# Performance work log

Measured on AMD Instinct MI355X. Metric: run time of the kernel, lower is better.

Reference implementation:

```python
import jax, jax.numpy as jnp
import numpy as np


def setup_inputs() -> dict:
    key = jax.random.key(0)
    k1, k2, k3, k4 = jax.random.split(key, 4)
    B, N, M, D = 4, 4096, 4096, 64
    x = jax.random.normal(k1, (B, N, D), dtype=jnp.float32)
    y = jax.random.normal(k2, (B, M, D), dtype=jnp.float32)
    mu = jax.random.normal(k3, (D, 1), dtype=jnp.float32)
    logs2diag = jax.random.normal(k4, (D,), dtype=jnp.float32) * 0.1
    return {"x": x, "y": y, "mu": mu, "logs2diag": logs2diag}


def reference(x, y, mu, logs2diag):
    # Diagonal scaling: x_ = x @ diag(exp(logs2diag)**0.5) == x * s_sqrt (broadcast)
    s_sqrt = jnp.exp(0.5 * logs2diag)  # [D]
    x_ = x * s_sqrt  # [B,N,D]
    y_ = y * s_sqrt  # [B,M,D]
    # cos term: M = x@mu - (y@mu)^T  -> [B,N,M]
    m_x = jnp.einsum('bnd,dk->bnk', x, mu)  # [B,N,1]
    m_y = jnp.einsum('bmd,dk->bmk', y, mu)  # [B,M,1]
    Mdiff = m_x - jnp.swapaxes(m_y, 1, 2)   # [B,N,M]
    # squared euclidean distance without sqrt (exp(-0.5*cdist^2))
    x2 = jnp.sum(x_ * x_, axis=-1, keepdims=True)      # [B,N,1]
    y2 = jnp.sum(y_ * y_, axis=-1, keepdims=True)      # [B,M,1]
    xy = jnp.einsum('bnd,bmd->bnm', x_, y_)            # [B,N,M]
    sqd = jnp.maximum(x2 + jnp.swapaxes(y2, 1, 2) - 2.0 * xy, 0.0)
    return jnp.cos(Mdiff) * jnp.exp(-0.5 * sqd)
```

## Files before the change

kernel.cpp:

```cpp
#include <hip/hip_runtime.h>
#include <math.h>

typedef __attribute__((ext_vector_type(8))) short short8;
typedef __attribute__((ext_vector_type(4))) float f32x4;

constexpr int D    = 64;
constexpr int BT_N = 64;
constexpr int BT_M = 512;
constexpr int NSUB = 8;

__device__ inline float fastcos_rev(float r) {
#if __has_builtin(__builtin_amdgcn_cosf)
    return __builtin_amdgcn_cosf(r);
#else
    return __cosf(r * 6.283185307179586f);
#endif
}
__device__ inline float fastsin_rev(float r) {
#if __has_builtin(__builtin_amdgcn_sinf)
    return __builtin_amdgcn_sinf(r);
#else
    return __sinf(r * 6.283185307179586f);
#endif
}

__device__ inline void split8(const float* v, short8& hi, short8& lo) {
    #pragma unroll
    for (int j = 0; j < 8; ++j) {
        unsigned u = __builtin_bit_cast(unsigned, v[j]);
        hi[j] = (short)(u >> 16);
        float hf = __builtin_bit_cast(float, u & 0xffff0000u);
        float r  = v[j] - hf;
        lo[j] = (short)(__builtin_bit_cast(unsigned, r) >> 16);
    }
}

__device__ inline void split1(float f, short& hi, short& lo) {
    unsigned u = __builtin_bit_cast(unsigned, f);
    hi = (short)(u >> 16);
    float hf = __builtin_bit_cast(float, u & 0xffff0000u);
    lo = (short)(__builtin_bit_cast(unsigned, f - hf) >> 16);
}

__global__ __launch_bounds__(256) void prep_kernel(
    const float* __restrict__ x, const float* __restrict__ y,
    const float* __restrict__ mu, const float* __restrict__ ls2,
    unsigned short* __restrict__ xh, unsigned short* __restrict__ xl,
    unsigned short* __restrict__ yh, unsigned short* __restrict__ yl,
    float4* __restrict__ xst, float4* __restrict__ yst,
    int BN, int BM)
{
    __shared__ float ss[D], sm[D];
    const int t = threadIdx.x;
    if (t < D) { ss[t] = __expf(0.5f * ls2[t]); sm[t] = mu[t]; }
    __syncthreads();

    const int gid = blockIdx.x * 256 + t;
    const int row = gid >> 3;
    const int sub = gid & 7;
    if (row >= BN + BM) return;

    const float* src;
    unsigned short *ph, *pl;
    float4* pst;
    int r;
    if (row < BN) { r = row;      src = x + (size_t)r * D; ph = xh; pl = xl; pst = xst; }
    else          { r = row - BN; src = y + (size_t)r * D; ph = yh; pl = yl; pst = yst; }

    const int k0 = sub * 8;
    float4 u0 = *(const float4*)(src + k0);
    float4 u1 = *(const float4*)(src + k0 + 4);
    const float4 m0 = *(const float4*)&sm[k0];
    const float4 m1 = *(const float4*)&sm[k0 + 4];
    const float4 s0 = *(const float4*)&ss[k0];
    const float4 s1 = *(const float4*)&ss[k0 + 4];

    float m = u0.x*m0.x + u0.y*m0.y + u0.z*m0.z + u0.w*m0.w
            + u1.x*m1.x + u1.y*m1.y + u1.z*m1.z + u1.w*m1.w;
    u0.x *= s0.x; u0.y *= s0.y; u0.z *= s0.z; u0.w *= s0.w;
    u1.x *= s1.x; u1.y *= s1.y; u1.z *= s1.z; u1.w *= s1.w;
    float h = u0.x*u0.x + u0.y*u0.y + u0.z*u0.z + u0.w*u0.w
            + u1.x*u1.x + u1.y*u1.y + u1.z*u1.z + u1.w*u1.w;

    m += __shfl_xor(m, 1); m += __shfl_xor(m, 2); m += __shfl_xor(m, 4);
    h += __shfl_xor(h, 1); h += __shfl_xor(h, 2); h += __shfl_xor(h, 4);

    if (sub == 0) {
        constexpr float INV2PI = 0.15915494309189535f;
        float rr = m * INV2PI;
        rr -= floorf(rr);
        pst[r] = (float4){0.5f * h, fastcos_rev(rr), fastsin_rev(rr), 0.f};
    }

    float v[8] = {u0.x, u0.y, u0.z, u0.w, u1.x, u1.y, u1.z, u1.w};
    short8 hi, lo;
    split8(v, hi, lo);
    const size_t o = (size_t)(r >> 4) * 1024 + (size_t)(sub * 16 + (r & 15)) * 8;
    *(short8*)(ph + o) = hi;
    *(short8*)(pl + o) = lo;
}

__device__ __forceinline__ void load_b(
    short8 (&bh)[2][2], short8 (&bl)[2][2],
    const unsigned short* __restrict__ ybh, const unsigned short* __restrict__ ybl,
    int st)
{
    #pragma unroll
    for (int kc = 0; kc < 2; ++kc)
        #pragma unroll
        for (int j = 0; j < 2; ++j) {
            const size_t o = (size_t)st * 4096 + j * 1024 + kc * 512;
            bh[kc][j] = *(const short8*)(ybh + o);
            bl[kc][j] = *(const short8*)(ybl + o);
        }
}

__device__ __forceinline__ void compute_store(
    const short8 (&ah)[2][2], const short8 (&al)[2][2],
    const short8 (&exA)[2],
    const short8 (&bh)[2][2], const short8 (&bl)[2][2],
    const float4* __restrict__ stB,
    const float (&say)[2][4], const float (&saz)[2][4],
    float* __restrict__ outb, int M, int st, int wc, int l15, int lg)
{
    short8 exB[2];
    #pragma unroll
    for (int j = 0; j < 2; ++j) {
        const float hy = -stB[st * 64 + wc * 32 + j * 16 + l15].x;
        short hh, hl;
        split1(hy, hh, hl);
        short8 v = (short8){0,0,0,0,0,0,0,0};
        if (lg == 0) { v[0] = (short)0x3f80; v[1] = (short)0x3f80; v[2] = hh; v[3] = hl; }
        exB[j] = v;
    }

    f32x4 acc[2][2];
    #pragma unroll
    for (int i = 0; i < 2; ++i)
        #pragma unroll
        for (int j = 0; j < 2; ++j)
            acc[i][j] = (f32x4){0.f, 0.f, 0.f, 0.f};

    #pragma unroll
    for (int kc = 0; kc < 2; ++kc)
        #pragma unroll
        for (int i = 0; i < 2; ++i)
            #pragma unroll
            for (int j = 0; j < 2; ++j) {
                acc[i][j] = __builtin_amdgcn_mfma_f32_16x16x32_bf16(ah[kc][i], bh[kc][j], acc[i][j], 0, 0, 0);
                acc[i][j] = __builtin_amdgcn_mfma_f32_16x16x32_bf16(ah[kc][i], bl[kc][j], acc[i][j], 0, 0, 0);
                acc[i][j] = __builtin_amdgcn_mfma_f32_16x16x32_bf16(al[kc][i], bh[kc][j], acc[i][j], 0, 0, 0);
            }
    #pragma unroll
    for (int i = 0; i < 2; ++i)
        #pragma unroll
        for (int j = 0; j < 2; ++j)
            acc[i][j] = __builtin_amdgcn_mfma_f32_16x16x32_bf16(exA[i], exB[j], acc[i][j], 0, 0, 0);

    const float4 sb0 = stB[st * 64 + wc * 32 + l15];
    const float4 sb1 = stB[st * 64 + wc * 32 + 16 + l15];
    #pragma unroll
    for (int i = 0; i < 2; ++i)
        #pragma unroll
        for (int q = 0; q < 4; ++q) {
            {
                const float cv = say[i][q] * sb0.y + saz[i][q] * sb0.z;
                outb[(size_t)(i * 16 + q) * M + st * 64] = cv * __expf(acc[i][0][q]);
            }
            {
                const float cv = say[i][q] * sb1.y + saz[i][q] * sb1.z;
                outb[(size_t)(i * 16 + q) * M + st * 64 + 16] = cv * __expf(acc[i][1][q]);
            }
        }
}

__global__ __launch_bounds__(256) void main_kernel(
    const unsigned short* __restrict__ xh, const unsigned short* __restrict__ xl,
    const unsigned short* __restrict__ yh, const unsigned short* __restrict__ yl,
    const float4* __restrict__ xst, const float4* __restrict__ yst,
    float* __restrict__ out, int N, int M)
{
    __shared__ float4 stA[BT_N], stB[BT_M];

    const int b  = blockIdx.z;
    const int n0 = blockIdx.y * BT_N;
    const int m0 = blockIdx.x * BT_M;
    const int t  = threadIdx.x;

    stB[t]       = yst[(size_t)b * M + m0 + t];
    stB[t + 256] = yst[(size_t)b * M + m0 + 256 + t];
    if (t < BT_N) stA[t] = xst[(size_t)b * N + n0 + t];
    __syncthreads();

    const int w = t >> 6, lane = t & 63;
    const int wr = w >> 1, wc = w & 1;
    const int l15 = lane & 15, lg = lane >> 4;

    const size_t tA0 = (((size_t)b * N + n0) >> 4) + wr * 2;
    const size_t tB0 = (((size_t)b * M + m0) >> 4) + wc * 2;
    const unsigned short* xbh = xh + tA0 * 1024 + (size_t)lane * 8;
    const unsigned short* xbl = xl + tA0 * 1024 + (size_t)lane * 8;
    const unsigned short* ybh = yh + tB0 * 1024 + (size_t)lane * 8;
    const unsigned short* ybl = yl + tB0 * 1024 + (size_t)lane * 8;

    short8 ah[2][2], al[2][2];
    #pragma unroll
    for (int kc = 0; kc < 2; ++kc)
        #pragma unroll
        for (int i = 0; i < 2; ++i) {
            ah[kc][i] = *(const short8*)(xbh + i * 1024 + kc * 512);
            al[kc][i] = *(const short8*)(xbl + i * 1024 + kc * 512);
        }

    short8 exA[2];
    #pragma unroll
    for (int i = 0; i < 2; ++i) {
        const float hx = -stA[wr * 32 + i * 16 + l15].x;
        short hh, hl;
        split1(hx, hh, hl);
        short8 v = (short8){0,0,0,0,0,0,0,0};
        if (lg == 0) { v[0] = hh; v[1] = hl; v[2] = (short)0x3f80; v[3] = (short)0x3f80; }
        exA[i] = v;
    }

    float say[2][4], saz[2][4];
    #pragma unroll
    for (int i = 0; i < 2; ++i)
        #pragma unroll
        for (int q = 0; q < 4; ++q) {
            const float4 v = stA[wr * 32 + i * 16 + lg * 4 + q];
            say[i][q] = v.y; saz[i][q] = v.z;
        }

    float* outb = out + ((size_t)b * N + n0 + wr * 32 + lg * 4) * (size_t)M
                + m0 + wc * 32 + l15;

    short8 bh0[2][2], bl0[2][2], bh1[2][2], bl1[2][2];
    load_b(bh0, bl0, ybh, ybl, 0);
    #pragma unroll
    for (int st = 0; st < NSUB; st += 2) {
        if (st + 1 < NSUB) load_b(bh1, bl1, ybh, ybl, st + 1);
        compute_store(ah, al, exA, bh0, bl0, stB, say, saz, outb, M, st, wc, l15, lg);
        if (st + 2 < NSUB) load_b(bh0, bl0, ybh, ybl, st + 2);
        if (st + 1 < NSUB)
            compute_store(ah, al, exA, bh1, bl1, stB, say, saz, outb, M, st + 1, wc, l15, lg);
    }
}

constexpr int FTILE = 64;
constexpr int FPAD  = 68;
__global__ __launch_bounds__(256) void fallback_kernel(
    const float* __restrict__ x, const float* __restrict__ y,
    const float* __restrict__ mu, const float* __restrict__ ls2,
    float* __restrict__ out, int N, int M)
{
    __shared__ float xs[FTILE][FPAD];
    __shared__ float ys[FTILE][FPAD];
    __shared__ float musc[D];
    __shared__ float sx2[FTILE], smx[FTILE], sy2[FTILE], smy[FTILE];

    const int b  = blockIdx.z;
    const int n0 = blockIdx.y * FTILE;
    const int m0 = blockIdx.x * FTILE;
    const int t  = threadIdx.x;
    const int cc = t & 15, rr = t >> 4, c4 = cc * 4;

    const float s0 = __expf(0.5f * ls2[c4+0]);
    const float s1 = __expf(0.5f * ls2[c4+1]);
    const float s2 = __expf(0.5f * ls2[c4+2]);
    const float s3 = __expf(0.5f * ls2[c4+3]);
    const float* xb = x + ((size_t)b * N + n0) * D;
    const float* yb = y + ((size_t)b * M + m0) * D;

    #pragma unroll
    for (int r = 0; r < 4; ++r) {
        const int row = rr * 4 + r;
        const float4 vx = *(const float4*)(xb + row * D + c4);
        const float4 vy = *(const float4*)(yb + row * D + c4);
        xs[row][c4+0] = vx.x * s0; xs[row][c4+1] = vx.y * s1;
        xs[row][c4+2] = vx.z * s2; xs[row][c4+3] = vx.w * s3;
        ys[row][c4+0] = vy.x * s0; ys[row][c4+1] = vy.y * s1;
        ys[row][c4+2] = vy.z * s2; ys[row][c4+3] = vy.w * s3;
    }
    if (t < D) musc[t] = mu[t] * __expf(-0.5f * ls2[t]);
    __syncthreads();

    if (t < 64) {
        float a2 = 0.f, am = 0.f;
        #pragma unroll
        for (int d4 = 0; d4 < D; d4 += 4) {
            const float4 v = *(const float4*)&xs[t][d4];
            const float4 m4 = *(const float4*)&musc[d4];
            a2 += v.x*v.x + v.y*v.y + v.z*v.z + v.w*v.w;
            am += v.x*m4.x + v.y*m4.y + v.z*m4.z + v.w*m4.w;
        }
        sx2[t] = a2; smx[t] = am;
    } else if (t < 128) {
        const int r2 = t - 64;
        float a2 = 0.f, am = 0.f;
        #pragma unroll
        for (int d4 = 0; d4 < D; d4 += 4) {
            const float4 v = *(const float4*)&ys[r2][d4];
            const float4 m4 = *(const float4*)&musc[d4];
            a2 += v.x*v.x + v.y*v.y + v.z*v.z + v.w*v.w;
            am += v.x*m4.x + v.y*m4.y + v.z*m4.z + v.w*m4.w;
        }
        sy2[r2] = a2; smy[r2] = am;
    }
    __syncthreads();

    const int tx = t & 15, ty = t >> 4;
    float acc[4][4] = {};
    #pragma unroll
    for (int d = 0; d < D; d += 4) {
        float4 a4[4], b4[4];
        #pragma unroll
        for (int i = 0; i < 4; ++i) a4[i] = *(const float4*)&xs[ty + 16*i][d];
        #pragma unroll
        for (int j = 0; j < 4; ++j) b4[j] = *(const float4*)&ys[tx + 16*j][d];
        #pragma unroll
        for (int i = 0; i < 4; ++i)
            #pragma unroll
            for (int j = 0; j < 4; ++j) {
                acc[i][j] += a4[i].x*b4[j].x + a4[i].y*b4[j].y
                           + a4[i].z*b4[j].z + a4[i].w*b4[j].w;
            }
    }

    constexpr float INV2PI = 0.15915494309189535f;
    #pragma unroll
    for (int i = 0; i < 4; ++i) {
        const int nl = ty + 16*i;
        float* orow = out + ((size_t)(b * N + n0 + nl)) * (size_t)M + m0;
        const float x2v = sx2[nl], mxv = smx[nl];
        #pragma unroll
        for (int j = 0; j < 4; ++j) {
            const int ml = tx + 16*j;
            float sqd = fmaxf(x2v + sy2[ml] - 2.0f*acc[i][j], 0.0f);
            float r = (mxv - smy[ml]) * INV2PI;
            r -= floorf(r);
            orow[ml] = fastcos_rev(r) * __expf(-0.5f * sqd);
        }
    }
}

extern "C" void kernel_launch(void* const* d_in, const int* in_sizes, int n_in,
                              void* d_out, int out_size, void* d_ws, size_t ws_size,
                              hipStream_t stream)
{
    const float* x   = (const float*)d_in[0];
    const float* y   = (const float*)d_in[1];
    const float* mu  = (const float*)d_in[2];
    const float* ls2 = (const float*)d_in[3];
    float* out = (float*)d_out;

    const int Dd = in_sizes[3];
    const long long BN = in_sizes[0] / Dd;
    const long long BM = in_sizes[1] / Dd;
    const int B = (int)((BN * BM) / (long long)out_size);
    const int N = (int)(BN / B);
    const int M = (int)(BM / B);

    const size_t need = (size_t)(BN + BM) * D * 2 * 2
                      + (size_t)(BN + BM) * sizeof(float4);

    if (ws_size >= need && (N % BT_N) == 0 && (M % BT_M) == 0) {
        unsigned short* xh = (unsigned short*)d_ws;
        unsigned short* xl = xh + (size_t)BN * D;
        unsigned short* yh = xl + (size_t)BN * D;
        unsigned short* yl = yh + (size_t)BM * D;
        float4* xst = (float4*)(yl + (size_t)BM * D);
        float4* yst = xst + BN;

        const long long rows8 = (BN + BM) * 8;
        hipLaunchKernelGGL(prep_kernel, dim3((int)((rows8 + 255) / 256)), dim3(256), 0, stream,
                           x, y, mu, ls2, xh, xl, yh, yl, xst, yst, (int)BN, (int)BM);
        hipLaunchKernelGGL(main_kernel, dim3(M / BT_M, N / BT_N, B), dim3(256), 0, stream,
                           xh, xl, yh, yl, xst, yst, out, N, M);
    } else {
        hipLaunchKernelGGL(fallback_kernel, dim3(M / FTILE, N / FTILE, B), dim3(256), 0, stream,
                           x, y, mu, ls2, out, N, M);
    }
}
```

Measured before the change: 65.24 us.

## Stage output tile in LDS and write coalesced float4 rows; halve M tile

```diff
diff --git a/kernel.cpp b/kernel.cpp
--- a/kernel.cpp
+++ b/kernel.cpp
@@ -6,8 +6,8 @@
 
 constexpr int D    = 64;
 constexpr int BT_N = 64;
-constexpr int BT_M = 512;
-constexpr int NSUB = 8;
+constexpr int BT_M = 256;
+constexpr int NSUB = 4;
 
 __device__ inline float fastcos_rev(float r) {
 #if __has_builtin(__builtin_amdgcn_cosf)
@@ -115,13 +115,13 @@
         }
 }
 
-__device__ __forceinline__ void compute_store(
+__device__ __forceinline__ void compute_to_lds(
     const short8 (&ah)[2][2], const short8 (&al)[2][2],
     const short8 (&exA)[2],
     const short8 (&bh)[2][2], const short8 (&bl)[2][2],
     const float4* __restrict__ stB,
     const float (&say)[2][4], const float (&saz)[2][4],
-    float* __restrict__ outb, int M, int st, int wc, int l15, int lg)
+    float* __restrict__ ldsT, int st, int wr, int wc, int l15, int lg)
 {
     short8 exB[2];
     #pragma unroll
@@ -159,17 +159,19 @@
 
     const float4 sb0 = stB[st * 64 + wc * 32 + l15];
     const float4 sb1 = stB[st * 64 + wc * 32 + 16 + l15];
+    const int mbase = wc * 32 + st * 64 + l15;
     #pragma unroll
     for (int i = 0; i < 2; ++i)
         #pragma unroll
         for (int q = 0; q < 4; ++q) {
+            const int nl = wr * 32 + i * 16 + lg * 4 + q;
             {
                 const float cv = say[i][q] * sb0.y + saz[i][q] * sb0.z;
-                outb[(size_t)(i * 16 + q) * M + st * 64] = cv * __expf(acc[i][0][q]);
+                ldsT[nl * BT_M + mbase] = cv * __expf(acc[i][0][q]);
             }
             {
                 const float cv = say[i][q] * sb1.y + saz[i][q] * sb1.z;
-                outb[(size_t)(i * 16 + q) * M + st * 64 + 16] = cv * __expf(acc[i][1][q]);
+                ldsT[nl * BT_M + mbase + 16] = cv * __expf(acc[i][1][q]);
             }
         }
 }
@@ -180,6 +182,7 @@
     const float4* __restrict__ xst, const float4* __restrict__ yst,
     float* __restrict__ out, int N, int M)
 {
+    extern __shared__ float ldsT[];
     __shared__ float4 stA[BT_N], stB[BT_M];
 
     const int b  = blockIdx.z;
@@ -187,8 +190,7 @@
     const int m0 = blockIdx.x * BT_M;
     const int t  = threadIdx.x;
 
-    stB[t]       = yst[(size_t)b * M + m0 + t];
-    stB[t + 256] = yst[(size_t)b * M + m0 + 256 + t];
+    stB[t] = yst[(size_t)b * M + m0 + t];
     if (t < BT_N) stA[t] = xst[(size_t)b * N + n0 + t];
     __syncthreads();
 
@@ -232,18 +234,24 @@
             say[i][q] = v.y; saz[i][q] = v.z;
         }
 
-    float* outb = out + ((size_t)b * N + n0 + wr * 32 + lg * 4) * (size_t)M
-                + m0 + wc * 32 + l15;
-
     short8 bh0[2][2], bl0[2][2], bh1[2][2], bl1[2][2];
     load_b(bh0, bl0, ybh, ybl, 0);
-    #pragma unroll
-    for (int st = 0; st < NSUB; st += 2) {
-        if (st + 1 < NSUB) load_b(bh1, bl1, ybh, ybl, st + 1);
-        compute_store(ah, al, exA, bh0, bl0, stB, say, saz, outb, M, st, wc, l15, lg);
-        if (st + 2 < NSUB) load_b(bh0, bl0, ybh, ybl, st + 2);
-        if (st + 1 < NSUB)
-            compute_store(ah, al, exA, bh1, bl1, stB, say, saz, outb, M, st + 1, wc, l15, lg);
+    load_b(bh1, bl1, ybh, ybl, 1);
+    compute_to_lds(ah, al, exA, bh0, bl0, stB, say, saz, ldsT, 0, wr, wc, l15, lg);
+    load_b(bh0, bl0, ybh, ybl, 2);
+    compute_to_lds(ah, al, exA, bh1, bl1, stB, say, saz, ldsT, 1, wr, wc, l15, lg);
+    load_b(bh1, bl1, ybh, ybl, 3);
+    compute_to_lds(ah, al, exA, bh0, bl0, stB, say, saz, ldsT, 2, wr, wc, l15, lg);
+    compute_to_lds(ah, al, exA, bh1, bl1, stB, say, saz, ldsT, 3, wr, wc, l15, lg);
+
+    __syncthreads();
+
+    const float4* ltf = (const float4*)ldsT;
+    float* outw = out + ((size_t)b * N + n0 + w * 16) * (size_t)M + m0 + lane * 4;
+    #pragma unroll
+    for (int rr = 0; rr < 16; ++rr) {
+        const float4 v = ltf[(w * 16 + rr) * (BT_M / 4) + lane];
+        *(float4*)(outw + (size_t)rr * M) = v;
     }
 }
 
@@ -375,7 +383,8 @@
         const long long rows8 = (BN + BM) * 8;
         hipLaunchKernelGGL(prep_kernel, dim3((int)((rows8 + 255) / 256)), dim3(256), 0, stream,
                            x, y, mu, ls2, xh, xl, yh, yl, xst, yst, (int)BN, (int)BM);
-        hipLaunchKernelGGL(main_kernel, dim3(M / BT_M, N / BT_N, B), dim3(256), 0, stream,
+        const size_t shmem = (size_t)BT_N * BT_M * sizeof(float);
+        hipLaunchKernelGGL(main_kernel, dim3(M / BT_M, N / BT_N, B), dim3(256), shmem, stream,
                            xh, xl, yh, yl, xst, yst, out, N, M);
     } else {
         hipLaunchKernelGGL(fallback_kernel, dim3(M / FTILE, N / FTILE, B), dim3(256), 0, stream,
```

After: 69.55 us. +6.6%, slower.
